# Performance work log

Hardware: AMD Instinct MI355X
Metric: run time of the kernel (lower is better)

Reference implementation:

```python
import jax, jax.numpy as jnp
import numpy as np
from jax import lax

H, W = 2048, 2048
KS = 3            # spatial NMS / centroid kernel size
EPS_NMS = 1e-5    # NMS3d eps (threshold=0 branch)
EPS_DIV = 1e-8
BORDER = 1        # int(mrSize=1.0)


def _grid_weights():
    # generate_3dgrid(3, 3, 3) centered: coords = linspace(-k/2+1, k/2, k) = [-0.5, 0.5, 1.5]
    c = np.linspace(-KS / 2 + 1, KS / 2, KS).astype(np.float32)
    g2 = np.stack([np.repeat(c, KS), np.tile(c, KS)], 1)                              # [9,2] (y,x), y-major
    g3 = np.concatenate([np.repeat(c, KS * KS)[:, None], np.tile(g2, (KS, 1))], 1)    # [27,3] (z,y,x)
    # grid.t().view(3,3,3,3): out-channel c holds coordinate c over the 3x3x3 cube (OIHW)
    return jnp.asarray(g3.T.reshape(3, 3, KS, KS))


def _border_mask():
    m = np.ones((H, W), np.float32)
    m[:BORDER] = 0; m[H - BORDER:] = 0; m[:, :BORDER] = 0; m[:, W - BORDER:] = 0
    return jnp.asarray(m)


def setup_inputs() -> dict:
    key = jax.random.key(0)
    k1, k2, k3, k4 = jax.random.split(key, 4)
    return {
        "low": jax.random.uniform(k1, (1, 1, H, W), jnp.float32),
        "cur": jax.random.uniform(k2, (1, 1, H, W), jnp.float32),
        "high": jax.random.uniform(k3, (1, 1, H, W), jnp.float32),
        "aff_resp": jax.random.normal(k4, (1, 4, H, W), jnp.float32),
        "octaveMap": jnp.zeros((1, 1, H, W), jnp.float32),
        "num_features": 4096,
    }


def _core(low, cur, high, aff_resp, octaveMap, num_features):
    resp3d = jnp.concatenate([low, cur, high], axis=1)  # [1,3,H,W] scale cube
    # MaxPool3d(kernel=3, stride=1, padding=(0,1,1)) over (scale,H,W) -> [1,1,H,W]
    mp = lax.reduce_window(resp3d, -jnp.inf, lax.max,
                           (1, 3, 3, 3), (1, 1, 1, 1),
                           [(0, 0), (0, 0), (1, 1), (1, 1)])
    nms = (resp3d - mp + EPS_NMS > 0).astype(resp3d.dtype) * resp3d  # broadcast over 3 scales
    # keep only the center scale, zero 1px border, mask already-taken octave positions
    nmsed = nms[:, 1:2] * _border_mask() * (1.0 - octaveMap)          # [1,1,H,W]
    vals, idxs = lax.top_k(nmsed.reshape(-1), num_features)          # fixed-k selection branch
    # centroid fit: coordinate-weighted 3x3x3 sums / mass via conv2d over the 3 scale channels
    gw = _grid_weights()
    num = lax.conv_general_dilated(resp3d, gw, (1, 1), [(1, 1), (1, 1)])
    den = lax.conv_general_dilated(resp3d, jnp.ones((3, 3, KS, KS), resp3d.dtype),
                                   (1, 1), [(1, 1), (1, 1)])
    sc = num / (den + EPS_DIV)  # [1,3,H,W] = (scale, dy, dx)
    yy, xx = jnp.meshgrid(jnp.arange(H, dtype=sc.dtype), jnp.arange(W, dtype=sc.dtype), indexing="ij")
    sc = jnp.stack([sc[0, 0], sc[0, 1] + yy, sc[0, 2] + xx], 0).reshape(3, -1).T  # [H*W,3]
    sc = sc[idxs] / jnp.array([float(min(H, W)), float(H), float(W)], sc.dtype)   # normalize (s,y,x)
    A = aff_resp.reshape(4, -1).T[idxs].reshape(-1, 2, 2)   # gather per-keypoint affine
    A = sc[:, 0][:, None, None] * A                          # scale * A
    center_xy = jnp.stack([sc[:, 2], sc[:, 1]], axis=1)[:, :, None]  # (x, y) column
    lafs = jnp.concatenate([A, center_xy], axis=2)           # [K,2,3] LAFs
    return vals, lafs, nmsed


def reference(low, cur, high, aff_resp, octaveMap, num_features):
    vals, lafs, nmsed = _core(low, cur, high, aff_resp, octaveMap, num_features)
    octave_new = (octaveMap + nmsed).astype(jnp.uint8)  # updated octave occupancy map
    return vals, lafs, octave_new
```

## Files before the change

kernel.cpp:

```cpp
#include <hip/hip_runtime.h>
#include <cstdint>
#include <cstddef>

#define HH 2048
#define WW 2048
#define NPIX (HH * WW)
#define EPS_NMS 1e-5f
#define EPS_DIV 1e-8f
#define NEG_INF (-3.402823466e+38f)
#define ROWS 4
#define LCAP 1024
#define SG_CAP 8192
#define NBIN 2048
#define SEL_BLOCKS 64

typedef unsigned long long u64;


__device__ __forceinline__ float max3(float a, float b, float c) {
    return fmaxf(a, fmaxf(b, c));
}

__device__ __forceinline__ unsigned int aload(const unsigned int* p) {
    return __hip_atomic_load(p, __ATOMIC_RELAXED, __HIP_MEMORY_SCOPE_AGENT);
}

__device__ __forceinline__ void gbar(unsigned int* ctr) {
    __syncthreads();
    if (threadIdx.x == 0) {
        __threadfence();
        atomicAdd(ctr, 1u);
        while (aload(ctr) < (unsigned int)SEL_BLOCKS) {}
        __threadfence();
    }
    __syncthreads();
}

__global__ __launch_bounds__(256) void nms_map_kernel(
    const float* __restrict__ low, const float* __restrict__ cur,
    const float* __restrict__ high, const float* __restrict__ oct,
    float* __restrict__ oct_out, float* __restrict__ vals_out, int n7k,
    u64* __restrict__ cand, unsigned int* __restrict__ cnt, unsigned int cap)
{
    __shared__ unsigned int lcount, lbase;
    __shared__ u64 lcand[LCAP];

    const int tid = threadIdx.x;
    const int lane = tid & 63;
    const int x4 = blockIdx.x * 1024 + tid * 4;
    const int y0 = blockIdx.y * ROWS;
    if (tid == 0) lcount = 0u;

    if (blockIdx.y == 0) {
        int n4 = n7k >> 2;
        float4* vz = (float4*)vals_out;
        for (int i = blockIdx.x * 256 + tid; i < n4; i += gridDim.x * 256)
            vz[i] = make_float4(0.f, 0.f, 0.f, 0.f);
    }
    __syncthreads();

    float4 L[ROWS + 2], C[ROWS + 2], Hi[ROWS + 2];
    float eL[ROWS + 2][3], eR[ROWS + 2][3];
    #pragma unroll
    for (int r = 0; r < ROWS + 2; ++r) {
        int t = y0 - 1 + r;
        bool valid = (t >= 0) && (t < HH);
        int jj = valid ? (t * WW + x4) : 0;
        if (valid) {
            L[r]  = *(const float4*)(low + jj);
            C[r]  = *(const float4*)(cur + jj);
            Hi[r] = *(const float4*)(high + jj);
        } else {
            L[r] = C[r] = Hi[r] = make_float4(NEG_INF, NEG_INF, NEG_INF, NEG_INF);
        }
        bool doL = valid && (lane == 0) && (x4 > 0);
        bool doR = valid && (lane == 63) && (x4 + 4 < WW);
        eL[r][0] = doL ? low[jj - 1]  : NEG_INF;
        eL[r][1] = doL ? cur[jj - 1]  : NEG_INF;
        eL[r][2] = doL ? high[jj - 1] : NEG_INF;
        eR[r][0] = doR ? low[jj + 4]  : NEG_INF;
        eR[r][1] = doR ? cur[jj + 4]  : NEG_INF;
        eR[r][2] = doR ? high[jj + 4] : NEG_INF;
    }
    float4 O[ROWS];
    #pragma unroll
    for (int j = 0; j < ROWS; ++j)
        O[j] = *(const float4*)(oct + (y0 + j) * WW + x4);

    float4 hz[ROWS + 2], cv[ROWS + 2];
    #pragma unroll
    for (int r = 0; r < ROWS + 2; ++r) {
        int t = y0 - 1 + r;
        bool valid = (t >= 0) && (t < HH);
        float4 z;
        z.x = max3(L[r].x, C[r].x, Hi[r].x);
        z.y = max3(L[r].y, C[r].y, Hi[r].y);
        z.z = max3(L[r].z, C[r].z, Hi[r].z);
        z.w = max3(L[r].w, C[r].w, Hi[r].w);
        float zeL = max3(eL[r][0], eL[r][1], eL[r][2]);
        float zeR = max3(eR[r][0], eR[r][1], eR[r][2]);
        float zl = __shfl_up(z.w, 1, 64);
        float zr = __shfl_down(z.x, 1, 64);
        if (lane == 0)  zl = zeL;
        if (lane == 63) zr = zeR;
        if (valid) {
            hz[r].x = max3(zl,  z.x, z.y);
            hz[r].y = max3(z.x, z.y, z.z);
            hz[r].z = max3(z.y, z.z, z.w);
            hz[r].w = max3(z.z, z.w, zr);
            cv[r] = C[r];
        } else {
            hz[r] = make_float4(NEG_INF, NEG_INF, NEG_INF, NEG_INF);
            cv[r] = make_float4(0.f, 0.f, 0.f, 0.f);
        }
    }

    #pragma unroll
    for (int j = 0; j < ROWS; ++j) {
        int y = y0 + j;
        int idx = y * WW + x4;
        float4 o = O[j];
        float4 c1 = cv[j + 1];
        bool yin = (y > 0) && (y < HH - 1);
        float4 ov;
        #define DO_COMP(comp, i)  {                                               \
            float m = max3(hz[j].comp, hz[j + 1].comp, hz[j + 2].comp);           \
            int xg = x4 + (i);                                                    \
            bool interior = yin && (xg > 0) && (xg < WW - 1);                     \
            float nm = (((c1.comp - m + EPS_NMS) > 0.0f) && interior)             \
                       ? c1.comp * (1.0f - o.comp) : 0.0f;                        \
            ov.comp = (float)((unsigned char)(o.comp + nm));                      \
            if (nm > 0.0f) {                                                      \
                unsigned int p = atomicAdd(&lcount, 1u);                          \
                if (p < LCAP)                                                     \
                    lcand[p] = (((u64)__float_as_uint(nm)) << 32)                 \
                               | (unsigned int)(~(idx + (i)));                    \
            }                                                                     \
        }
        DO_COMP(x, 0) DO_COMP(y, 1) DO_COMP(z, 2) DO_COMP(w, 3)
        #undef DO_COMP
        *(float4*)(oct_out + idx) = ov;
    }

    __syncthreads();
    unsigned int c = lcount < LCAP ? lcount : LCAP;
    if (tid == 0) lbase = atomicAdd(cnt, c);
    __syncthreads();
    unsigned int base = lbase;
    for (unsigned int i = tid; i < c; i += 256) {
        unsigned int p = base + i;
        if (p < cap) cand[p] = lcand[i];
    }
}

__global__ __launch_bounds__(256) void select_kernel(
    const u64* __restrict__ cand, u64* __restrict__ SG,
    unsigned int* __restrict__ cnt, unsigned int* __restrict__ hist,
    unsigned int cap, int K)
{
    __shared__ unsigned int h[NBIN];
    __shared__ unsigned int s[256];
    __shared__ unsigned int sh_prefix, sh_remk;
    __shared__ unsigned int lc, lb;
    __shared__ u64 buf[2048];
    const int tid = threadIdx.x;
    const int bid = blockIdx.x;
    unsigned int* bar = cnt + 16;
    unsigned int n = cnt[0]; if (n > cap) n = cap;
    const unsigned int stride = SEL_BLOCKS * 256;

    int gtid = bid * 256 + tid;
    if (gtid < NBIN) hist[gtid] = 0u;
    for (int i = tid; i < NBIN; i += 256) h[i] = 0u;
    __syncthreads();

    for (unsigned int i = bid * 256 + tid; i < n; i += stride)
        atomicAdd(&h[(unsigned int)(cand[i] >> 53)], 1u);
    gbar(&bar[0]);
    for (int i = tid; i < NBIN; i += 256) { unsigned int v = h[i]; if (v) atomicAdd(&hist[i], v); }
    gbar(&bar[1]);

    if (bid == 0) {
        unsigned int bins[8], csum = 0;
        #pragma unroll
        for (int i = 0; i < 8; ++i) { bins[i] = aload(&hist[tid * 8 + i]); csum += bins[i]; }
        s[tid] = csum;
        __syncthreads();
        for (int off = 1; off < 256; off <<= 1) {
            unsigned int v = (tid + off < 256) ? s[tid + off] : 0u;
            __syncthreads(); s[tid] += v; __syncthreads();
        }
        unsigned int remk = (unsigned int)K;
        unsigned int incl = s[tid], excl = incl - csum, total = s[0];
        if (incl >= remk && excl < remk) {
            unsigned int cum = excl; int b = 7;
            for (; b > 0; --b) { cum += bins[b]; if (cum >= remk) break; }
            if (cum < remk) cum += bins[0];
            sh_prefix = (unsigned int)(tid * 8 + b);
            sh_remk   = remk - (cum - bins[b]);
        }
        if (tid == 0 && total < remk) { sh_prefix = 0u; sh_remk = remk; }
        __syncthreads();
        for (int i = tid; i < NBIN; i += 256) hist[i] = 0u;
        __syncthreads();
        if (tid == 0) atomicExch(&cnt[3], sh_prefix);
    }
    gbar(&bar[2]);

    unsigned int prefix = aload(&cnt[3]);
    for (int i = tid; i < NBIN; i += 256) h[i] = 0u;
    __syncthreads();
    for (unsigned int i = bid * 256 + tid; i < n; i += stride) {
        unsigned int k32 = (unsigned int)(cand[i] >> 32);
        if ((k32 >> 21) == prefix) atomicAdd(&h[(k32 >> 10) & (NBIN - 1u)], 1u);
    }
    __syncthreads();
    for (int i = tid; i < NBIN; i += 256) { unsigned int v = h[i]; if (v) atomicAdd(&hist[i], v); }
    gbar(&bar[3]);

    if (bid == 0) {
        unsigned int bins[8], csum = 0;
        #pragma unroll
        for (int i = 0; i < 8; ++i) { bins[i] = aload(&hist[tid * 8 + i]); csum += bins[i]; }
        s[tid] = csum;
        __syncthreads();
        for (int off = 1; off < 256; off <<= 1) {
            unsigned int v = (tid + off < 256) ? s[tid + off] : 0u;
            __syncthreads(); s[tid] += v; __syncthreads();
        }
        unsigned int remk = sh_remk, pfx = sh_prefix;
        unsigned int incl = s[tid], excl = incl - csum, total = s[0];
        __shared__ unsigned int sh_T;
        if (tid == 0) sh_T = pfx << 11;
        __syncthreads();
        if (incl >= remk && excl < remk) {
            unsigned int cum = excl; int b = 7;
            for (; b > 0; --b) { cum += bins[b]; if (cum >= remk) break; }
            if (cum < remk) cum += bins[0];
            sh_T = (pfx << 11) | (unsigned int)(tid * 8 + b);
        }
        __syncthreads();
        if (tid == 0) atomicExch(&cnt[3], sh_T);
    }
    gbar(&bar[4]);

    unsigned int T = aload(&cnt[3]);
    if (tid == 0) lc = 0u;
    __syncthreads();
    for (unsigned int i = bid * 256 + tid; i < n; i += stride) {
        u64 key = cand[i];
        if ((unsigned int)(key >> 42) >= T) {
            unsigned int p = atomicAdd(&lc, 1u);
            if (p < 2048u) buf[p] = key;
        }
    }
    __syncthreads();
    unsigned int c = lc < 2048u ? lc : 2048u;
    if (tid == 0) lb = atomicAdd(&cnt[1], c);
    __syncthreads();
    unsigned int base = lb;
    for (unsigned int i = tid; i < c; i += 256) {
        unsigned int p = base + i;
        if (p < SG_CAP) SG[p] = buf[i];
    }
}

__global__ __launch_bounds__(256) void rank_finalize_kernel(
    const u64* __restrict__ SG, const unsigned int* __restrict__ cnt,
    const float* __restrict__ low, const float* __restrict__ cur,
    const float* __restrict__ high, const float* __restrict__ aff,
    float* __restrict__ out, int K)
{
    unsigned int m = cnt[1]; if (m > SG_CAP) m = SG_CAP;
    unsigned int wave = threadIdx.x >> 6;
    unsigned int lane = threadIdx.x & 63u;
    unsigned int e = blockIdx.x * 4 + wave;
    if (e >= m) return;
    u64 my = SG[e];

    unsigned int rank = 0;
    for (unsigned int j = lane; j < m; j += 64)
        rank += (unsigned)(SG[j] > my);
    #pragma unroll
    for (int off = 32; off > 0; off >>= 1)
        rank += __shfl_down(rank, off, 64);
    if (lane != 0) return;
    if (rank >= (unsigned int)K) return;

    float val = __uint_as_float((unsigned int)(my >> 32));
    unsigned int idx = ~((unsigned int)my);
    out[rank] = val;
    float* laf = out + K + (size_t)rank * 6;
    int y = (int)(idx >> 11), x = (int)(idx & (WW - 1));
    const float ccw[3] = {-0.5f, 0.5f, 1.5f};
    float den = 0.0f, nz = 0.0f, ny = 0.0f, nx = 0.0f;
    #pragma unroll
    for (int dy = -1; dy <= 1; ++dy) {
        int yy = y + dy;
        if (yy < 0 || yy >= HH) continue;
        #pragma unroll
        for (int dx = -1; dx <= 1; ++dx) {
            int xx = x + dx;
            if (xx < 0 || xx >= WW) continue;
            int jj = yy * WW + xx;
            float v0 = low[jj], v1 = cur[jj], v2 = high[jj];
            float ssum = v0 + v1 + v2;
            den += ssum;
            nz += -0.5f * v0 + 0.5f * v1 + 1.5f * v2;
            ny += ccw[dy + 1] * ssum;
            nx += ccw[dx + 1] * ssum;
        }
    }
    float inv = 1.0f / (den + EPS_DIV);
    float s_n = (nz * inv) * (1.0f / 2048.0f);
    float y_n = (ny * inv + (float)y) * (1.0f / 2048.0f);
    float x_n = (nx * inv + (float)x) * (1.0f / 2048.0f);
    float a0 = aff[idx], a1 = aff[NPIX + idx], a2 = aff[2 * NPIX + idx], a3 = aff[3 * NPIX + idx];
    laf[0] = s_n * a0; laf[1] = s_n * a1; laf[2] = x_n;
    laf[3] = s_n * a2; laf[4] = s_n * a3; laf[5] = y_n;
}

extern "C" void kernel_launch(void* const* d_in, const int* in_sizes, int n_in,
                              void* d_out, int out_size, void* d_ws, size_t ws_size,
                              hipStream_t stream) {
    const float* low  = (const float*)d_in[0];
    const float* cur  = (const float*)d_in[1];
    const float* high = (const float*)d_in[2];
    const float* aff  = (const float*)d_in[3];
    const float* oct  = (const float*)d_in[4];
    int K = (out_size - NPIX) / 7;
    float* out = (float*)d_out;

    char* ws = (char*)d_ws;
    unsigned int* cnt  = (unsigned int*)ws;
    unsigned int* hist = (unsigned int*)(ws + 128);
    u64* SG            = (u64*)(ws + 16384);
    const size_t cand_off = 81920;
    u64* cand          = (u64*)(ws + cand_off);
    size_t cap_sz = ws_size > cand_off ? (ws_size - cand_off) / 8 : 0;
    if (cap_sz > (size_t)NPIX) cap_sz = (size_t)NPIX;
    unsigned int cap = (unsigned int)cap_sz;

    hipMemsetAsync(ws, 0, 128, stream);

    dim3 gb(WW / 1024, HH / ROWS, 1);
    nms_map_kernel<<<gb, 256, 0, stream>>>(low, cur, high, oct, out + (size_t)7 * K,
                                           out, 7 * K, cand, cnt, cap);
    select_kernel<<<SEL_BLOCKS, 256, 0, stream>>>(cand, SG, cnt, hist, cap, K);
    rank_finalize_kernel<<<SG_CAP / 4, 256, 0, stream>>>(SG, cnt, low, cur, high, aff, out, K);
}
```

Before: 212.0 us.

## Stream NMS rows through a double buffer and batch rank counting in LDS

The NMS kernel now processes 8 rows per block, loading input rows through a two-slot rolling buffer that computes each row's horizontal max once and reuses it across the sliding window. Next-row loads are issued before the current row is computed, and the local candidate capacity is doubled to match. The rank kernel stages the whole candidate list in 64 KB of shared memory and has each wave rank 8 keys per pass, so global re-reads are replaced by LDS reads. The risks are lower occupancy from the large LDS use and fewer NMS blocks.

```diff
diff --git a/kernel.cpp b/kernel.cpp
--- a/kernel.cpp
+++ b/kernel.cpp
@@ -8,11 +8,12 @@
 #define EPS_NMS 1e-5f
 #define EPS_DIV 1e-8f
 #define NEG_INF (-3.402823466e+38f)
-#define ROWS 4
-#define LCAP 1024
+#define ROWS 8
+#define LCAP 2048
 #define SG_CAP 8192
 #define NBIN 2048
 #define SEL_BLOCKS 64
+#define RB_ELEMS 32
 
 typedef unsigned long long u64;
 
@@ -59,76 +60,78 @@
     }
     __syncthreads();
 
-    float4 L[ROWS + 2], C[ROWS + 2], Hi[ROWS + 2];
-    float eL[ROWS + 2][3], eR[ROWS + 2][3];
-    #pragma unroll
-    for (int r = 0; r < ROWS + 2; ++r) {
-        int t = y0 - 1 + r;
-        bool valid = (t >= 0) && (t < HH);
-        int jj = valid ? (t * WW + x4) : 0;
-        if (valid) {
-            L[r]  = *(const float4*)(low + jj);
-            C[r]  = *(const float4*)(cur + jj);
-            Hi[r] = *(const float4*)(high + jj);
-        } else {
-            L[r] = C[r] = Hi[r] = make_float4(NEG_INF, NEG_INF, NEG_INF, NEG_INF);
-        }
-        bool doL = valid && (lane == 0) && (x4 > 0);
-        bool doR = valid && (lane == 63) && (x4 + 4 < WW);
-        eL[r][0] = doL ? low[jj - 1]  : NEG_INF;
-        eL[r][1] = doL ? cur[jj - 1]  : NEG_INF;
-        eL[r][2] = doL ? high[jj - 1] : NEG_INF;
-        eR[r][0] = doR ? low[jj + 4]  : NEG_INF;
-        eR[r][1] = doR ? cur[jj + 4]  : NEG_INF;
-        eR[r][2] = doR ? high[jj + 4] : NEG_INF;
-    }
-    float4 O[ROWS];
-    #pragma unroll
-    for (int j = 0; j < ROWS; ++j)
-        O[j] = *(const float4*)(oct + (y0 + j) * WW + x4);
-
-    float4 hz[ROWS + 2], cv[ROWS + 2];
-    #pragma unroll
-    for (int r = 0; r < ROWS + 2; ++r) {
-        int t = y0 - 1 + r;
-        bool valid = (t >= 0) && (t < HH);
-        float4 z;
-        z.x = max3(L[r].x, C[r].x, Hi[r].x);
-        z.y = max3(L[r].y, C[r].y, Hi[r].y);
-        z.z = max3(L[r].z, C[r].z, Hi[r].z);
-        z.w = max3(L[r].w, C[r].w, Hi[r].w);
-        float zeL = max3(eL[r][0], eL[r][1], eL[r][2]);
-        float zeR = max3(eR[r][0], eR[r][1], eR[r][2]);
-        float zl = __shfl_up(z.w, 1, 64);
-        float zr = __shfl_down(z.x, 1, 64);
-        if (lane == 0)  zl = zeL;
-        if (lane == 63) zr = zeR;
-        if (valid) {
-            hz[r].x = max3(zl,  z.x, z.y);
-            hz[r].y = max3(z.x, z.y, z.z);
-            hz[r].z = max3(z.y, z.z, z.w);
-            hz[r].w = max3(z.z, z.w, zr);
-            cv[r] = C[r];
-        } else {
-            hz[r] = make_float4(NEG_INF, NEG_INF, NEG_INF, NEG_INF);
-            cv[r] = make_float4(0.f, 0.f, 0.f, 0.f);
-        }
-    }
+    float4 Lb[2], Cb[2], Hb[2], Ob[2];
+    float eLl[2], eLc[2], eLh[2], eRl[2], eRc[2], eRh[2];
+
+    #define ISSUE(t, slot) {                                                      \
+        int tt = (t);                                                             \
+        if (tt >= 0 && tt < HH) {                                                 \
+            int jj = tt * WW + x4;                                                \
+            Lb[slot] = *(const float4*)(low  + jj);                               \
+            Cb[slot] = *(const float4*)(cur  + jj);                               \
+            Hb[slot] = *(const float4*)(high + jj);                               \
+            bool doL = (lane == 0)  && (x4 > 0);                                  \
+            bool doR = (lane == 63) && (x4 + 4 < WW);                             \
+            eLl[slot] = doL ? low[jj - 1]  : NEG_INF;                             \
+            eLc[slot] = doL ? cur[jj - 1]  : NEG_INF;                             \
+            eLh[slot] = doL ? high[jj - 1] : NEG_INF;                             \
+            eRl[slot] = doR ? low[jj + 4]  : NEG_INF;                             \
+            eRc[slot] = doR ? cur[jj + 4]  : NEG_INF;                             \
+            eRh[slot] = doR ? high[jj + 4] : NEG_INF;                             \
+        } else {                                                                  \
+            Lb[slot] = Cb[slot] = Hb[slot] =                                      \
+                make_float4(NEG_INF, NEG_INF, NEG_INF, NEG_INF);                  \
+            eLl[slot] = eLc[slot] = eLh[slot] = NEG_INF;                          \
+            eRl[slot] = eRc[slot] = eRh[slot] = NEG_INF;                          \
+        }                                                                         \
+    }
+
+    #define CONSUME(slot, hzO, cvO) {                                             \
+        float4 l = Lb[slot], c = Cb[slot], hh = Hb[slot];                         \
+        float4 z;                                                                 \
+        z.x = max3(l.x, c.x, hh.x);                                               \
+        z.y = max3(l.y, c.y, hh.y);                                               \
+        z.z = max3(l.z, c.z, hh.z);                                               \
+        z.w = max3(l.w, c.w, hh.w);                                               \
+        float zeL = max3(eLl[slot], eLc[slot], eLh[slot]);                        \
+        float zeR = max3(eRl[slot], eRc[slot], eRh[slot]);                        \
+        float zl = __shfl_up(z.w, 1, 64);                                         \
+        float zr = __shfl_down(z.x, 1, 64);                                       \
+        if (lane == 0)  zl = zeL;                                                 \
+        if (lane == 63) zr = zeR;                                                 \
+        hzO.x = max3(zl,  z.x, z.y);                                              \
+        hzO.y = max3(z.x, z.y, z.z);                                              \
+        hzO.z = max3(z.y, z.z, z.w);                                              \
+        hzO.w = max3(z.z, z.w, zr);                                               \
+        cvO = c;                                                                  \
+    }
+
+    float4 hzA, hzB, hzC, cvB, cvC, cvT;
+    ISSUE(y0 - 1, 0)
+    ISSUE(y0,     1)
+    Ob[0] = *(const float4*)(oct + y0 * WW + x4);
+    CONSUME(0, hzA, cvT)
+    ISSUE(y0 + 1, 0)
+    CONSUME(1, hzB, cvB)
 
     #pragma unroll
     for (int j = 0; j < ROWS; ++j) {
         int y = y0 + j;
+        ISSUE(y + 2, (j + 1) & 1)
+        if (j + 1 < ROWS)
+            Ob[(j + 1) & 1] = *(const float4*)(oct + (y + 1) * WW + x4);
+        CONSUME(j & 1, hzC, cvC)
+
         int idx = y * WW + x4;
-        float4 o = O[j];
-        float4 c1 = cv[j + 1];
+        float4 o = Ob[j & 1];
         bool yin = (y > 0) && (y < HH - 1);
         float4 ov;
         #define DO_COMP(comp, i)  {                                               \
-            float m = max3(hz[j].comp, hz[j + 1].comp, hz[j + 2].comp);           \
+            float m = max3(hzA.comp, hzB.comp, hzC.comp);                         \
             int xg = x4 + (i);                                                    \
             bool interior = yin && (xg > 0) && (xg < WW - 1);                     \
-            float nm = (((c1.comp - m + EPS_NMS) > 0.0f) && interior)             \
-                       ? c1.comp * (1.0f - o.comp) : 0.0f;                        \
+            float nm = (((cvB.comp - m + EPS_NMS) > 0.0f) && interior)            \
+                       ? cvB.comp * (1.0f - o.comp) : 0.0f;                       \
             ov.comp = (float)((unsigned char)(o.comp + nm));                      \
             if (nm > 0.0f) {                                                      \
                 unsigned int p = atomicAdd(&lcount, 1u);                          \
@@ -140,7 +143,10 @@
         DO_COMP(x, 0) DO_COMP(y, 1) DO_COMP(z, 2) DO_COMP(w, 3)
         #undef DO_COMP
         *(float4*)(oct_out + idx) = ov;
-    }
+        hzA = hzB; hzB = hzC; cvB = cvC;
+    }
+    #undef ISSUE
+    #undef CONSUME
 
     __syncthreads();
     unsigned int c = lcount < LCAP ? lcount : LCAP;
@@ -271,24 +277,47 @@
     const float* __restrict__ high, const float* __restrict__ aff,
     float* __restrict__ out, int K)
 {
+    __shared__ u64 s[SG_CAP];
+    __shared__ unsigned int rnk[RB_ELEMS];
     unsigned int m = cnt[1]; if (m > SG_CAP) m = SG_CAP;
-    unsigned int wave = threadIdx.x >> 6;
-    unsigned int lane = threadIdx.x & 63u;
-    unsigned int e = blockIdx.x * 4 + wave;
+    unsigned int base = blockIdx.x * RB_ELEMS;
+    if (base >= m) return;
+    for (unsigned int i = threadIdx.x; i < m; i += 256) s[i] = SG[i];
+    __syncthreads();
+
+    unsigned int wave = threadIdx.x >> 6, lane = threadIdx.x & 63u;
+    u64 my[8];
+    unsigned int r[8];
+    #pragma unroll
+    for (int i = 0; i < 8; ++i) {
+        unsigned int e = base + wave * 8 + i;
+        my[i] = (e < m) ? s[e] : ~0ull;
+        r[i] = 0u;
+    }
+    for (unsigned int j = lane; j < m; j += 64) {
+        u64 key = s[j];
+        #pragma unroll
+        for (int i = 0; i < 8; ++i) r[i] += (unsigned)(key > my[i]);
+    }
+    #pragma unroll
+    for (int i = 0; i < 8; ++i) {
+        #pragma unroll
+        for (int off = 32; off > 0; off >>= 1)
+            r[i] += __shfl_down(r[i], off, 64);
+        if (lane == 0) rnk[wave * 8 + i] = r[i];
+    }
+    __syncthreads();
+
+    int i = threadIdx.x;
+    if (i >= RB_ELEMS) return;
+    unsigned int e = base + (unsigned int)i;
     if (e >= m) return;
-    u64 my = SG[e];
-
-    unsigned int rank = 0;
-    for (unsigned int j = lane; j < m; j += 64)
-        rank += (unsigned)(SG[j] > my);
-    #pragma unroll
-    for (int off = 32; off > 0; off >>= 1)
-        rank += __shfl_down(rank, off, 64);
-    if (lane != 0) return;
+    unsigned int rank = rnk[i];
     if (rank >= (unsigned int)K) return;
-
-    float val = __uint_as_float((unsigned int)(my >> 32));
-    unsigned int idx = ~((unsigned int)my);
+    u64 my_key = s[e];
+
+    float val = __uint_as_float((unsigned int)(my_key >> 32));
+    unsigned int idx = ~((unsigned int)my_key);
     out[rank] = val;
     float* laf = out + K + (size_t)rank * 6;
     int y = (int)(idx >> 11), x = (int)(idx & (WW - 1));
@@ -347,5 +376,5 @@
     nms_map_kernel<<<gb, 256, 0, stream>>>(low, cur, high, oct, out + (size_t)7 * K,
                                            out, 7 * K, cand, cnt, cap);
     select_kernel<<<SEL_BLOCKS, 256, 0, stream>>>(cand, SG, cnt, hist, cap, K);
-    rank_finalize_kernel<<<SG_CAP / 4, 256, 0, stream>>>(SG, cnt, low, cur, high, aff, out, K);
-}
+    rank_finalize_kernel<<<SG_CAP / RB_ELEMS, 256, 0, stream>>>(SG, cnt, low, cur, high, aff, out, K);
+}
```

Result: faster. 203.7 us (-3.9%).

## Stage survivors in LDS and rank 32 keys per block in rank_finalize

Applied to the files above, without the earlier changes.

The rank kernel now copies the survivor key array into shared memory once per block, and each wave ranks eight keys at a time against it, so one LDS read is reused for several comparisons instead of every wave streaming the global array for a single key. This cuts the block count from SG_CAP/4 to SG_CAP/32. The NMS map kernel also switches to 2 rows per block with a smaller local candidate capacity, which gives more, smaller blocks. The 64 KB LDS buffer per block limits occupancy, and the smaller LCAP may overflow more often on dense rows.

```diff
diff --git a/kernel.cpp b/kernel.cpp
--- a/kernel.cpp
+++ b/kernel.cpp
@@ -8,11 +8,12 @@
 #define EPS_NMS 1e-5f
 #define EPS_DIV 1e-8f
 #define NEG_INF (-3.402823466e+38f)
-#define ROWS 4
-#define LCAP 1024
+#define ROWS 2
+#define LCAP 512
 #define SG_CAP 8192
 #define NBIN 2048
 #define SEL_BLOCKS 64
+#define RB_ELEMS 32
 
 typedef unsigned long long u64;
 
@@ -271,24 +272,47 @@
     const float* __restrict__ high, const float* __restrict__ aff,
     float* __restrict__ out, int K)
 {
+    __shared__ u64 s[SG_CAP];
+    __shared__ unsigned int rnk[RB_ELEMS];
     unsigned int m = cnt[1]; if (m > SG_CAP) m = SG_CAP;
-    unsigned int wave = threadIdx.x >> 6;
-    unsigned int lane = threadIdx.x & 63u;
-    unsigned int e = blockIdx.x * 4 + wave;
+    unsigned int base = blockIdx.x * RB_ELEMS;
+    if (base >= m) return;
+    for (unsigned int i = threadIdx.x; i < m; i += 256) s[i] = SG[i];
+    __syncthreads();
+
+    unsigned int wave = threadIdx.x >> 6, lane = threadIdx.x & 63u;
+    u64 my[8];
+    unsigned int r[8];
+    #pragma unroll
+    for (int i = 0; i < 8; ++i) {
+        unsigned int e = base + wave * 8 + i;
+        my[i] = (e < m) ? s[e] : ~0ull;
+        r[i] = 0u;
+    }
+    for (unsigned int j = lane; j < m; j += 64) {
+        u64 key = s[j];
+        #pragma unroll
+        for (int i = 0; i < 8; ++i) r[i] += (unsigned)(key > my[i]);
+    }
+    #pragma unroll
+    for (int i = 0; i < 8; ++i) {
+        #pragma unroll
+        for (int off = 32; off > 0; off >>= 1)
+            r[i] += __shfl_down(r[i], off, 64);
+        if (lane == 0) rnk[wave * 8 + i] = r[i];
+    }
+    __syncthreads();
+
+    int i = threadIdx.x;
+    if (i >= RB_ELEMS) return;
+    unsigned int e = base + (unsigned int)i;
     if (e >= m) return;
-    u64 my = SG[e];
-
-    unsigned int rank = 0;
-    for (unsigned int j = lane; j < m; j += 64)
-        rank += (unsigned)(SG[j] > my);
-    #pragma unroll
-    for (int off = 32; off > 0; off >>= 1)
-        rank += __shfl_down(rank, off, 64);
-    if (lane != 0) return;
+    unsigned int rank = rnk[i];
     if (rank >= (unsigned int)K) return;
-
-    float val = __uint_as_float((unsigned int)(my >> 32));
-    unsigned int idx = ~((unsigned int)my);
+    u64 my_key = s[e];
+
+    float val = __uint_as_float((unsigned int)(my_key >> 32));
+    unsigned int idx = ~((unsigned int)my_key);
     out[rank] = val;
     float* laf = out + K + (size_t)rank * 6;
     int y = (int)(idx >> 11), x = (int)(idx & (WW - 1));
@@ -347,5 +371,5 @@
     nms_map_kernel<<<gb, 256, 0, stream>>>(low, cur, high, oct, out + (size_t)7 * K,
                                            out, 7 * K, cand, cnt, cap);
     select_kernel<<<SEL_BLOCKS, 256, 0, stream>>>(cand, SG, cnt, hist, cap, K);
-    rank_finalize_kernel<<<SG_CAP / 4, 256, 0, stream>>>(SG, cnt, low, cur, high, aff, out, K);
-}
+    rank_finalize_kernel<<<SG_CAP / RB_ELEMS, 256, 0, stream>>>(SG, cnt, low, cur, high, aff, out, K);
+}
```

Measured after the change: 219.6 us. 1.04x slower.
